# Performance work log

Hardware: AMD Instinct MI355X
Metric: run time of the kernel (lower is better)

## Reference

```python
import math
import jax, jax.numpy as jnp
import numpy as np

NHEAD = 8


def setup_inputs() -> dict:
    key = jax.random.key(0)
    ks = jax.random.split(key, 16)
    B, S, M, Ss, Ksn, D = 8, 512, 8, 16, 16, 512
    f32 = jnp.float32
    w_scale = 0.05
    return {
        "q_temporal": jax.random.normal(ks[0], (B, S, M, D), f32),
        "k_temporal": jax.random.normal(ks[1], (B, S, M, D), f32),
        "v_temporal": jax.random.normal(ks[2], (B, S, M, D), f32),
        "q_static": jax.random.normal(ks[3], (B, Ss, D), f32),
        "k_static": jax.random.normal(ks[4], (B, Ksn, D), f32),
        "v_static": jax.random.normal(ks[5], (B, Ksn, D), f32),
        "mask_temporal": jax.random.randint(ks[6], (B, S, M), 0, 2).astype(jnp.int32),
        "mask_static": jax.random.randint(ks[7], (B, Ksn), 0, 2).astype(jnp.int32),
        "Wq": jax.random.normal(ks[8], (D, D), f32) * w_scale,
        "bq": jax.random.normal(ks[9], (D,), f32) * w_scale,
        "Wk": jax.random.normal(ks[10], (D, D), f32) * w_scale,
        "bk": jax.random.normal(ks[11], (D,), f32) * w_scale,
        "Wv": jax.random.normal(ks[12], (D, D), f32) * w_scale,
        "bv": jax.random.normal(ks[13], (D,), f32) * w_scale,
        "Wo": jax.random.normal(ks[14], (D, D), f32) * w_scale,
        "bo": jax.random.normal(ks[15], (D,), f32) * w_scale,
    }


def reference(q_temporal, k_temporal, v_temporal, q_static, k_static, v_static,
              mask_temporal, mask_static, Wq, bq, Wk, bk, Wv, bv, Wo, bo):
    B, S, M, D = q_temporal.shape
    dh = D // NHEAD
    scale = 1.0 / math.sqrt(dh)
    SM = S * M

    def lin(x, W, b):
        return x @ W + b

    def h5(x):  # [B,S,M,D] -> [B,H,S,M,dh]
        b, s, m, d = x.shape
        return x.reshape(b, s, m, NHEAD, dh).transpose(0, 3, 1, 2, 4)

    def h4(x):  # [B,N,D] -> [B,H,N,dh]
        b, n, d = x.shape
        return x.reshape(b, n, NHEAD, dh).transpose(0, 2, 1, 3)

    # additive masks: 1 -> 0 (keep), 0 -> -inf
    m_t = jnp.where(mask_temporal == 1, 0.0, -jnp.inf)  # [B,S,M]
    m_s = jnp.where(mask_static == 1, 0.0, -jnp.inf)    # [B,Ks]

    # shared static-key/value heads: [B,H,Ks,dh]
    Ks_h = h4(lin(k_static, Wk, bk))
    Vs_h = h4(lin(v_static, Wv, bv))

    # ---- temporal side ----
    Qt = h5(lin(q_temporal, Wq, bq))   # [B,H,S,M,dh]
    Kt = h5(lin(k_temporal, Wk, bk))
    Vt = h5(lin(v_temporal, Wv, bv))
    qt_kt = jnp.einsum('bhsmd,bhsnd->bhsmn', Qt, Kt) * scale + m_t[:, None, :, None, :]   # [B,H,S,M,M]
    qt_ks = jnp.einsum('bhsmd,bhkd->bhsmk', Qt, Ks_h) * scale + m_s[:, None, None, None, :]  # [B,H,S,M,Ks]
    w_t = jax.nn.softmax(jnp.concatenate([qt_kt, qt_ks], axis=-1), axis=-1)  # [B,H,S,M,M+Ks]
    qkv_t = (jnp.einsum('bhsmn,bhsnd->bhsmd', w_t[..., :M], Vt)
             + jnp.einsum('bhsmk,bhkd->bhsmd', w_t[..., M:], Vs_h))          # [B,H,S,M,dh]
    out_t = lin(qkv_t.transpose(0, 2, 3, 1, 4).reshape(B, S, M, D), Wo, bo)  # [B,S,M,D]

    # ---- static side ----
    Qs = h4(lin(q_static, Wq, bq))                              # [B,H,Ss,dh]
    Kt_f = h4(lin(k_temporal.reshape(B, SM, D), Wk, bk))        # [B,H,S*M,dh]
    Vt_f = h4(lin(v_temporal.reshape(B, SM, D), Wv, bv))
    qs_kt = jnp.einsum('bhqd,bhnd->bhqn', Qs, Kt_f) * scale + m_t.reshape(B, 1, 1, SM)  # [B,H,Ss,S*M]
    qs_ks = jnp.einsum('bhqd,bhkd->bhqk', Qs, Ks_h) * scale + m_s[:, None, None, :]     # [B,H,Ss,Ks]
    w_s = jax.nn.softmax(jnp.concatenate([qs_kt, qs_ks], axis=-1), axis=-1)  # [B,H,Ss,S*M+Ks]
    qkv_s = (jnp.einsum('bhqn,bhnd->bhqd', w_s[..., :SM], Vt_f)
             + jnp.einsum('bhqk,bhkd->bhqd', w_s[..., SM:], Vs_h))           # [B,H,Ss,dh]
    Ss = qkv_s.shape[2]
    out_s = lin(qkv_s.transpose(0, 2, 1, 3).reshape(B, Ss, D), Wo, bo)       # [B,Ss,D]

    return (out_t, w_t, out_s, w_s)
```

## Files before the change

### kernel.cpp

```cpp
#include <hip/hip_runtime.h>
#include <hip/hip_bf16.h>

typedef __attribute__((ext_vector_type(8))) __bf16 bf16x8;
typedef __attribute__((ext_vector_type(4))) float f32x4;

__device__ __forceinline__ float b2f(unsigned short u) {
    unsigned int x = ((unsigned int)u) << 16;
    float f;
    __builtin_memcpy(&f, &x, 4);
    return f;
}
__device__ __forceinline__ unsigned short f2b(float f) {
    __hip_bfloat16 h = __float2bfloat16(f);
    unsigned short u;
    __builtin_memcpy(&u, &h, 2);
    return u;
}
union U4 { uint4 v; unsigned short u[8]; };

__global__ __launch_bounds__(256) void transpose512cvt(const float* __restrict__ in,
                                                       unsigned short* __restrict__ out)
{
    __shared__ float tile[32][33];
    int tx = threadIdx.x & 31, ty = threadIdx.x >> 5;
    int bx = blockIdx.x, by = blockIdx.y;
    #pragma unroll
    for (int i = 0; i < 32; i += 8)
        tile[ty + i][tx] = in[(size_t)(bx * 32 + ty + i) * 512 + by * 32 + tx];
    __syncthreads();
    #pragma unroll
    for (int i = 0; i < 32; i += 8)
        out[(size_t)(by * 32 + ty + i) * 512 + bx * 32 + tx] = f2b(tile[tx][ty + i]);
}

#define GPAD 40

template<bool AF32, int CMODE>
__global__ __launch_bounds__(256) void gemm128(
    const void* __restrict__ Av,
    const unsigned short* __restrict__ Bt,
    const float* __restrict__ bias,
    void* __restrict__ Cv,
    int M, int N)
{
    const int K = 512;
    __shared__ __align__(16) unsigned short As[128 * GPAD];
    __shared__ __align__(16) unsigned short Bs[128 * GPAD];

    int nblk = gridDim.x, bid = blockIdx.x;
    int wid = ((nblk & 7) == 0) ? ((bid & 7) * (nblk >> 3) + (bid >> 3)) : bid;
    int nt = N >> 7;
    int m0 = (wid / nt) * 128, n0 = (wid % nt) * 128;

    int t = threadIdx.x;
    int wave = t >> 6, lane = t & 63, quad = lane >> 4, l16 = lane & 15;
    int wr = wave >> 1, wc = wave & 1;

    f32x4 acc[4][4];
    #pragma unroll
    for (int i = 0; i < 4; ++i)
        #pragma unroll
        for (int j = 0; j < 4; ++j) acc[i][j] = (f32x4){0.f, 0.f, 0.f, 0.f};

    int r = t >> 1, half = (t & 1) * 16;
    const float* Ap32 = (const float*)Av + (size_t)(m0 + r) * K + half;
    const unsigned short* Ap16 = (const unsigned short*)Av + (size_t)(m0 + r) * K + half;
    const unsigned short* Bp = Bt + (size_t)(n0 + r) * K + half;

    float4 fa0, fa1, fa2, fa3;
    U4 ua0, ua1;
    uint4 fb0, fb1;

    auto LOADK = [&](int k0) {
        if constexpr (AF32) {
            const float4* p = (const float4*)(Ap32 + k0);
            fa0 = p[0]; fa1 = p[1]; fa2 = p[2]; fa3 = p[3];
        } else {
            ua0.v = *(const uint4*)(Ap16 + k0);
            ua1.v = *(const uint4*)(Ap16 + k0 + 8);
        }
        fb0 = *(const uint4*)(Bp + k0);
        fb1 = *(const uint4*)(Bp + k0 + 8);
    };
    auto STOREK = [&]() {
        U4 a0, a1;
        if constexpr (AF32) {
            a0.u[0]=f2b(fa0.x); a0.u[1]=f2b(fa0.y); a0.u[2]=f2b(fa0.z); a0.u[3]=f2b(fa0.w);
            a0.u[4]=f2b(fa1.x); a0.u[5]=f2b(fa1.y); a0.u[6]=f2b(fa1.z); a0.u[7]=f2b(fa1.w);
            a1.u[0]=f2b(fa2.x); a1.u[1]=f2b(fa2.y); a1.u[2]=f2b(fa2.z); a1.u[3]=f2b(fa2.w);
            a1.u[4]=f2b(fa3.x); a1.u[5]=f2b(fa3.y); a1.u[6]=f2b(fa3.z); a1.u[7]=f2b(fa3.w);
        } else {
            a0 = ua0; a1 = ua1;
        }
        *(uint4*)&As[r * GPAD + half] = a0.v;
        *(uint4*)&As[r * GPAD + half + 8] = a1.v;
        *(uint4*)&Bs[r * GPAD + half] = fb0;
        *(uint4*)&Bs[r * GPAD + half + 8] = fb1;
    };

    LOADK(0);
    for (int it = 0; it < 16; ++it) {
        __syncthreads();
        STOREK();
        __syncthreads();
        if (it < 15) LOADK((it + 1) * 32);
        bf16x8 af[4], bf[4];
        #pragma unroll
        for (int i = 0; i < 4; ++i)
            af[i] = *(const bf16x8*)&As[(wr * 64 + i * 16 + l16) * GPAD + quad * 8];
        #pragma unroll
        for (int j = 0; j < 4; ++j)
            bf[j] = *(const bf16x8*)&Bs[(wc * 64 + j * 16 + l16) * GPAD + quad * 8];
        #pragma unroll
        for (int i = 0; i < 4; ++i)
            #pragma unroll
            for (int j = 0; j < 4; ++j)
                acc[i][j] = __builtin_amdgcn_mfma_f32_16x16x32_bf16(af[i], bf[j], acc[i][j], 0, 0, 0);
    }
    #pragma unroll
    for (int i = 0; i < 4; ++i) {
        #pragma unroll
        for (int j = 0; j < 4; ++j) {
            int row = m0 + wr * 64 + i * 16 + quad * 4;
            int col = n0 + wc * 64 + j * 16 + l16;
            float bc = bias[col];
            #pragma unroll
            for (int ii = 0; ii < 4; ++ii) {
                float v = acc[i][j][ii] + bc;
                int R = row + ii;
                if constexpr (CMODE == 0) {
                    ((float*)Cv)[(size_t)R * N + col] = v;
                } else if constexpr (CMODE == 1) {
                    ((unsigned short*)Cv)[(size_t)R * N + col] = f2b(v);
                } else {
                    int bb = R >> 12, n = R & 4095, hh = col >> 6, d = col & 63;
                    ((unsigned short*)Cv)[(((size_t)bb * 8 + hh) * 4096 + n) * 64 + d] = f2b(v);
                }
            }
        }
    }
}

__global__ __launch_bounds__(512) void temporal_attn(
    const unsigned short* __restrict__ Qt, const unsigned short* __restrict__ KH,
    const unsigned short* __restrict__ VH, const unsigned short* __restrict__ Ksp,
    const unsigned short* __restrict__ Vsp,
    const int* __restrict__ mask_t, const int* __restrict__ mask_s,
    float* __restrict__ w_t_out, unsigned short* __restrict__ qkv_t)
{
    int blk = blockIdx.x;
    int b = blk >> 8, sp = blk & 255;
    int s0 = sp * 2;
    int t = threadIdx.x;
    int h = t >> 6, lane = t & 63, quad = lane >> 4, l16 = lane & 15;

    __shared__ __align__(16) unsigned short Vt[8][64 * 40];
    __shared__ __align__(16) unsigned short Pl[8][16 * 40];

    size_t bh = (size_t)(b * 8 + h);
    size_t tok0 = ((size_t)(b * 512 + s0)) * 8;

    {
        int r = lane & 31, dh = (lane >> 5) * 32;
        const unsigned short* src = (r < 16)
            ? VH + (bh * 4096 + (size_t)(s0 * 8 + r)) * 64 + dh
            : Vsp + ((size_t)(b * 16 + (r - 16))) * 512 + h * 64 + dh;
        U4 u[4];
        #pragma unroll
        for (int g = 0; g < 4; ++g) u[g].v = ((const uint4*)src)[g];
        unsigned short* dst = &Vt[h][0];
        #pragma unroll
        for (int g = 0; g < 4; ++g)
            #pragma unroll
            for (int ii = 0; ii < 8; ++ii)
                dst[(dh + g * 8 + ii) * 40 + r] = u[g].u[ii];
    }

    const unsigned short* qp = Qt + (tok0 + l16) * 512 + h * 64 + quad * 8;
    bf16x8 qf0 = *(const bf16x8*)qp;
    bf16x8 qf1 = *(const bf16x8*)(qp + 32);
    const unsigned short* kpt = KH + (bh * 4096 + (size_t)(s0 * 8 + l16)) * 64 + quad * 8;
    bf16x8 kt0 = *(const bf16x8*)kpt;
    bf16x8 kt1 = *(const bf16x8*)(kpt + 32);
    const unsigned short* kps = Ksp + ((size_t)(b * 16 + l16)) * 512 + h * 64 + quad * 8;
    bf16x8 ks0 = *(const bf16x8*)kps;
    bf16x8 ks1 = *(const bf16x8*)(kps + 32);

    f32x4 sc0 = (f32x4){0.f, 0.f, 0.f, 0.f};
    f32x4 sc1 = (f32x4){0.f, 0.f, 0.f, 0.f};
    sc0 = __builtin_amdgcn_mfma_f32_16x16x32_bf16(qf0, kt0, sc0, 0, 0, 0);
    sc0 = __builtin_amdgcn_mfma_f32_16x16x32_bf16(qf1, kt1, sc0, 0, 0, 0);
    sc1 = __builtin_amdgcn_mfma_f32_16x16x32_bf16(qf0, ks0, sc1, 0, 0, 0);
    sc1 = __builtin_amdgcn_mfma_f32_16x16x32_bf16(qf1, ks1, sc1, 0, 0, 0);

    float madd0 = mask_t[tok0 + l16] ? 0.f : -1e30f;
    bool v0 = ((quad < 2) == (l16 < 8));
    if (!v0) madd0 = -1e30f;
    float madd1 = mask_s[b * 16 + l16] ? 0.f : -1e30f;

    float w0[4], w1[4];
    #pragma unroll
    for (int i = 0; i < 4; ++i) {
        float a = sc0[i] * 0.125f + madd0;
        float c = sc1[i] * 0.125f + madd1;
        float mx = fmaxf(a, c);
        mx = fmaxf(mx, __shfl_xor(mx, 1));
        mx = fmaxf(mx, __shfl_xor(mx, 2));
        mx = fmaxf(mx, __shfl_xor(mx, 4));
        mx = fmaxf(mx, __shfl_xor(mx, 8));
        float e0 = __expf(a - mx), e1 = __expf(c - mx);
        float se = e0 + e1;
        se += __shfl_xor(se, 1);
        se += __shfl_xor(se, 2);
        se += __shfl_xor(se, 4);
        se += __shfl_xor(se, 8);
        float inv = 1.f / se;
        w0[i] = e0 * inv;
        w1[i] = e1 * inv;
    }

    int row0 = quad * 4;
    #pragma unroll
    for (int i = 0; i < 4; ++i) {
        int row = row0 + i;
        Pl[h][row * 40 + l16] = f2b(w0[i]);
        Pl[h][row * 40 + 16 + l16] = f2b(w1[i]);
        int s = s0 + (row >> 3), m = row & 7;
        size_t wb = ((((size_t)b * 8 + h) * 512 + s) * 8 + m) * 24;
        if (v0) w_t_out[wb + (l16 & 7)] = w0[i];
        w_t_out[wb + 8 + l16] = w1[i];
    }

    bf16x8 pa = *(const bf16x8*)&Pl[h][l16 * 40 + quad * 8];
    f32x4 oacc[4];
    #pragma unroll
    for (int j = 0; j < 4; ++j) {
        bf16x8 vb = *(const bf16x8*)&Vt[h][(j * 16 + l16) * 40 + quad * 8];
        oacc[j] = (f32x4){0.f, 0.f, 0.f, 0.f};
        oacc[j] = __builtin_amdgcn_mfma_f32_16x16x32_bf16(pa, vb, oacc[j], 0, 0, 0);
    }
    #pragma unroll
    for (int j = 0; j < 4; ++j)
        #pragma unroll
        for (int ii = 0; ii < 4; ++ii) {
            int row = quad * 4 + ii;
            qkv_t[(tok0 + row) * 512 + h * 64 + j * 16 + l16] = f2b(oacc[j][ii]);
        }
}

__global__ __launch_bounds__(256) void static_attn_s1(
    const unsigned short* __restrict__ Qsp, const unsigned short* __restrict__ KH,
    const unsigned short* __restrict__ VH, const unsigned short* __restrict__ Ksp,
    const unsigned short* __restrict__ Vsp,
    const int* __restrict__ mask_t, const int* __restrict__ mask_s,
    float* __restrict__ w_s, float* __restrict__ Ppart, float* __restrict__ Lpart)
{
    int blk = blockIdx.x;
    int bh = blk & 63, c = blk >> 6;
    int b = bh >> 3, h = bh & 7;
    __shared__ __align__(16) unsigned short Klds[32 * 72];
    __shared__ __align__(16) unsigned short Vlds[64 * 40];
    __shared__ __align__(16) unsigned short Plds[16 * 40];
    __shared__ float maskv[32];
    __shared__ float sL[2][16];
    int t = threadIdx.x, wave = t >> 6, lane = t & 63, quad = lane >> 4, l16 = lane & 15;

    bf16x8 qf0 = *(const bf16x8*)(Qsp + ((size_t)(b * 16 + l16)) * 512 + h * 64 + quad * 8);
    bf16x8 qf1 = *(const bf16x8*)(Qsp + ((size_t)(b * 16 + l16)) * 512 + h * 64 + 32 + quad * 8);

    f32x4 pacc = (f32x4){0.f, 0.f, 0.f, 0.f};
    float Lacc[4] = {0.f, 0.f, 0.f, 0.f};
    int d0 = wave * 16;
    int sub = wave >> 1;
    int sr = t >> 3, spart = t & 7;
    int s0 = c * 16, s1 = (c == 7) ? 129 : (s0 + 16);

    for (int st = s0; st < s1; ++st) {
        int key0 = st * 32;
        int kk = key0 + sr;
        uint4 kv = {0, 0, 0, 0}, vv = {0, 0, 0, 0};
        if (kk < 4096) {
            kv = *(const uint4*)(KH + (((size_t)bh) * 4096 + kk) * 64 + spart * 8);
            vv = *(const uint4*)(VH + (((size_t)bh) * 4096 + kk) * 64 + spart * 8);
        } else if (kk < 4112) {
            kv = *(const uint4*)(Ksp + ((size_t)(b * 16 + kk - 4096)) * 512 + h * 64 + spart * 8);
            vv = *(const uint4*)(Vsp + ((size_t)(b * 16 + kk - 4096)) * 512 + h * 64 + spart * 8);
        }
        __syncthreads();
        *(uint4*)&Klds[sr * 72 + spart * 8] = kv;
        {
            U4 u; u.v = vv;
            #pragma unroll
            for (int ii = 0; ii < 8; ++ii) Vlds[(spart * 8 + ii) * 40 + sr] = u.u[ii];
        }
        if (t < 32) {
            int k2 = key0 + t;
            float ma = -1e30f;
            if (k2 < 4096) ma = mask_t[b * 4096 + k2] ? 0.f : -1e30f;
            else if (k2 < 4112) ma = mask_s[b * 16 + k2 - 4096] ? 0.f : -1e30f;
            maskv[t] = ma;
        }
        __syncthreads();
        if ((wave & 1) == 0) {
            bf16x8 kf0 = *(const bf16x8*)&Klds[(sub * 16 + l16) * 72 + quad * 8];
            bf16x8 kf1 = *(const bf16x8*)&Klds[(sub * 16 + l16) * 72 + 32 + quad * 8];
            f32x4 sc = (f32x4){0.f, 0.f, 0.f, 0.f};
            sc = __builtin_amdgcn_mfma_f32_16x16x32_bf16(qf0, kf0, sc, 0, 0, 0);
            sc = __builtin_amdgcn_mfma_f32_16x16x32_bf16(qf1, kf1, sc, 0, 0, 0);
            float ma = maskv[sub * 16 + l16];
            size_t wbase = (((size_t)bh) * 16 + quad * 4) * 4112 + key0 + sub * 16 + l16;
            #pragma unroll
            for (int i = 0; i < 4; ++i) {
                float sv = sc[i] * 0.125f + ma;
                float w = __expf(sv);
                Lacc[i] += w;
                w_s[wbase + (size_t)i * 4112] = w;
                Plds[(quad * 4 + i) * 40 + sub * 16 + l16] = f2b(w);
            }
        }
        __syncthreads();
        bf16x8 pf = *(const bf16x8*)&Plds[l16 * 40 + quad * 8];
        bf16x8 vf = *(const bf16x8*)&Vlds[(d0 + l16) * 40 + quad * 8];
        pacc = __builtin_amdgcn_mfma_f32_16x16x32_bf16(pf, vf, pacc, 0, 0, 0);
    }

    if ((wave & 1) == 0) {
        #pragma unroll
        for (int i = 0; i < 4; ++i) {
            float v = Lacc[i];
            v += __shfl_xor(v, 1);
            v += __shfl_xor(v, 2);
            v += __shfl_xor(v, 4);
            v += __shfl_xor(v, 8);
            Lacc[i] = v;
        }
        if (l16 == 0) {
            #pragma unroll
            for (int i = 0; i < 4; ++i) sL[wave >> 1][quad * 4 + i] = Lacc[i];
        }
    }
    size_t pbase = ((size_t)(bh * 8 + c) * 16 + quad * 4) * 64 + d0 + l16;
    #pragma unroll
    for (int i = 0; i < 4; ++i) Ppart[pbase + (size_t)i * 64] = pacc[i];
    __syncthreads();
    if (t < 16) Lpart[(bh * 8 + c) * 16 + t] = sL[0][t] + sL[1][t];
}

__global__ __launch_bounds__(256) void static_attn_s4(
    const float* __restrict__ Ppart, const float* __restrict__ Lpart,
    float* __restrict__ w_s, unsigned short* __restrict__ qkvS)
{
    int bh = blockIdx.x, b = bh >> 3, h = bh & 7;
    __shared__ float invL[16];
    int t = threadIdx.x;
    if (t < 16) {
        float L = 0.f;
        #pragma unroll
        for (int cc = 0; cc < 8; ++cc) L += Lpart[(bh * 8 + cc) * 16 + t];
        invL[t] = 1.f / L;
    }
    __syncthreads();
    #pragma unroll
    for (int i = 0; i < 4; ++i) {
        int idx = t + i * 256;
        int q = idx >> 6, d = idx & 63;
        float s = 0.f;
        #pragma unroll
        for (int cc = 0; cc < 8; ++cc) s += Ppart[((size_t)(bh * 8 + cc) * 16 + q) * 64 + d];
        qkvS[((size_t)(b * 16 + q)) * 512 + h * 64 + d] = f2b(s * invL[q]);
    }
    size_t base = (size_t)bh * 16 * 4112;
    for (int q = 0; q < 16; ++q) {
        float il = invL[q];
        for (int kk = t; kk < 4112; kk += 256) w_s[base + q * 4112 + kk] *= il;
    }
}

extern "C" void kernel_launch(void* const* d_in, const int* in_sizes, int n_in,
                              void* d_out, int out_size, void* d_ws, size_t ws_size,
                              hipStream_t stream)
{
    const float* q_t = (const float*)d_in[0];
    const float* k_t = (const float*)d_in[1];
    const float* v_t = (const float*)d_in[2];
    const float* q_s = (const float*)d_in[3];
    const float* k_s = (const float*)d_in[4];
    const float* v_s = (const float*)d_in[5];
    const int* m_t = (const int*)d_in[6];
    const int* m_s = (const int*)d_in[7];
    const float* Wq = (const float*)d_in[8];
    const float* bq = (const float*)d_in[9];
    const float* Wk = (const float*)d_in[10];
    const float* bk = (const float*)d_in[11];
    const float* Wv = (const float*)d_in[12];
    const float* bv = (const float*)d_in[13];
    const float* Wo = (const float*)d_in[14];
    const float* bo = (const float*)d_in[15];

    char* ws = (char*)d_ws;
    size_t off = 0;
    auto alloc = [&](size_t bytes) {
        void* p = ws + off;
        off += (bytes + 255) & ~(size_t)255;
        return p;
    };
    const size_t WB = (size_t)512 * 512 * 2;
    const size_t TB = (size_t)32768 * 512 * 2;
    const size_t SB = (size_t)128 * 512 * 2;
    unsigned short* WqT = (unsigned short*)alloc(WB);
    unsigned short* WkT = (unsigned short*)alloc(WB);
    unsigned short* WvT = (unsigned short*)alloc(WB);
    unsigned short* WoT = (unsigned short*)alloc(WB);
    unsigned short* Qt   = (unsigned short*)alloc(TB);
    unsigned short* KH   = (unsigned short*)alloc(TB);
    unsigned short* VH   = (unsigned short*)alloc(TB);
    unsigned short* qkvT = (unsigned short*)alloc(TB);
    unsigned short* Qsp  = (unsigned short*)alloc(SB);
    unsigned short* Ksp  = (unsigned short*)alloc(SB);
    unsigned short* Vsp  = (unsigned short*)alloc(SB);
    unsigned short* qkvS = (unsigned short*)alloc(SB);
    float* Ppart = (float*)alloc((size_t)64 * 8 * 16 * 64 * 4);
    float* Lpart = (float*)alloc((size_t)64 * 8 * 16 * 4);

    float* out    = (float*)d_out;
    float* out_tp = out;
    float* w_t_o  = out + 16777216;
    float* out_sp = out + 23068672;
    float* w_s_o  = out + 23134208;

    transpose512cvt<<<dim3(16, 16), 256, 0, stream>>>(Wq, WqT);
    transpose512cvt<<<dim3(16, 16), 256, 0, stream>>>(Wk, WkT);
    transpose512cvt<<<dim3(16, 16), 256, 0, stream>>>(Wv, WvT);
    transpose512cvt<<<dim3(16, 16), 256, 0, stream>>>(Wo, WoT);

    gemm128<true, 1><<<dim3(1024), 256, 0, stream>>>(q_t, WqT, bq, Qt, 32768, 512);
    gemm128<true, 2><<<dim3(1024), 256, 0, stream>>>(k_t, WkT, bk, KH, 32768, 512);
    gemm128<true, 2><<<dim3(1024), 256, 0, stream>>>(v_t, WvT, bv, VH, 32768, 512);
    gemm128<true, 1><<<dim3(4),    256, 0, stream>>>(q_s, WqT, bq, Qsp, 128, 512);
    gemm128<true, 1><<<dim3(4),    256, 0, stream>>>(k_s, WkT, bk, Ksp, 128, 512);
    gemm128<true, 1><<<dim3(4),    256, 0, stream>>>(v_s, WvT, bv, Vsp, 128, 512);

    temporal_attn<<<2048, 512, 0, stream>>>(Qt, KH, VH, Ksp, Vsp, m_t, m_s, w_t_o, qkvT);
    static_attn_s1<<<512, 256, 0, stream>>>(Qsp, KH, VH, Ksp, Vsp, m_t, m_s, w_s_o, Ppart, Lpart);
    static_attn_s4<<<64, 256, 0, stream>>>(Ppart, Lpart, w_s_o, qkvS);

    gemm128<false, 0><<<dim3(1024), 256, 0, stream>>>(qkvT, WoT, bo, out_tp, 32768, 512);
    gemm128<false, 0><<<dim3(4),    256, 0, stream>>>(qkvS, WoT, bo, out_sp, 128, 512);
}
```

Baseline: 589.5 us.

## Batch QKV projection GEMMs and weight transposes into single launches, add register prefetch

Merges the four weight transpose kernels into one launch using blockIdx.z, and the three temporal (and three static) QKV projection GEMMs into one launch each using blockIdx.y to select a parameter set. The GEMM main loop now keeps two register staging buffers so global loads run two K-steps ahead of the MFMA compute. This cuts launch overhead and fills the GPU better for the tiny static GEMMs. In exchange, the output mode becomes a runtime branch instead of a template constant, and the extra staging registers may lower occupancy.

```diff
diff --git a/kernel.cpp b/kernel.cpp
--- a/kernel.cpp
+++ b/kernel.cpp
@@ -18,9 +18,17 @@
 }
 union U4 { uint4 v; unsigned short u[8]; };
 
-__global__ __launch_bounds__(256) void transpose512cvt(const float* __restrict__ in,
-                                                       unsigned short* __restrict__ out)
-{
+__global__ __launch_bounds__(256) void transpose512cvt4(
+    const float* __restrict__ i0, const float* __restrict__ i1,
+    const float* __restrict__ i2, const float* __restrict__ i3,
+    unsigned short* __restrict__ o0, unsigned short* __restrict__ o1,
+    unsigned short* __restrict__ o2, unsigned short* __restrict__ o3)
+{
+    const float* in = i0;
+    unsigned short* out = o0;
+    if (blockIdx.z == 1) { in = i1; out = o1; }
+    else if (blockIdx.z == 2) { in = i2; out = o2; }
+    else if (blockIdx.z == 3) { in = i3; out = o3; }
     __shared__ float tile[32][33];
     int tx = threadIdx.x & 31, ty = threadIdx.x >> 5;
     int bx = blockIdx.x, by = blockIdx.y;
@@ -35,14 +43,22 @@
 
 #define GPAD 40
 
-template<bool AF32, int CMODE>
+struct GemmSet {
+    const void* A;
+    const unsigned short* B;
+    const float* bias;
+    void* C;
+    int cmode;
+};
+
+template<bool AF32>
 __global__ __launch_bounds__(256) void gemm128(
-    const void* __restrict__ Av,
-    const unsigned short* __restrict__ Bt,
-    const float* __restrict__ bias,
-    void* __restrict__ Cv,
-    int M, int N)
-{
+    GemmSet s0, GemmSet s1, GemmSet s2, int M, int N)
+{
+    GemmSet S = s0;
+    if (blockIdx.y == 1) S = s1;
+    else if (blockIdx.y == 2) S = s2;
+
     const int K = 512;
     __shared__ __align__(16) unsigned short As[128 * GPAD];
     __shared__ __align__(16) unsigned short Bs[128 * GPAD];
@@ -63,15 +79,14 @@
         for (int j = 0; j < 4; ++j) acc[i][j] = (f32x4){0.f, 0.f, 0.f, 0.f};
 
     int r = t >> 1, half = (t & 1) * 16;
-    const float* Ap32 = (const float*)Av + (size_t)(m0 + r) * K + half;
-    const unsigned short* Ap16 = (const unsigned short*)Av + (size_t)(m0 + r) * K + half;
-    const unsigned short* Bp = Bt + (size_t)(n0 + r) * K + half;
-
-    float4 fa0, fa1, fa2, fa3;
-    U4 ua0, ua1;
-    uint4 fb0, fb1;
-
-    auto LOADK = [&](int k0) {
+    const float* Ap32 = (const float*)S.A + (size_t)(m0 + r) * K + half;
+    const unsigned short* Ap16 = (const unsigned short*)S.A + (size_t)(m0 + r) * K + half;
+    const unsigned short* Bp = S.B + (size_t)(n0 + r) * K + half;
+
+    float4 fa0, fa1, fa2, fa3; U4 ua0, ua1; uint4 fb0, fb1;
+    float4 ga0, ga1, ga2, ga3; U4 va0, va1; uint4 gb0, gb1;
+
+    auto LOAD0 = [&](int k0) {
         if constexpr (AF32) {
             const float4* p = (const float4*)(Ap32 + k0);
             fa0 = p[0]; fa1 = p[1]; fa2 = p[2]; fa3 = p[3];
@@ -82,28 +97,44 @@
         fb0 = *(const uint4*)(Bp + k0);
         fb1 = *(const uint4*)(Bp + k0 + 8);
     };
-    auto STOREK = [&]() {
+    auto LOAD1 = [&](int k0) {
+        if constexpr (AF32) {
+            const float4* p = (const float4*)(Ap32 + k0);
+            ga0 = p[0]; ga1 = p[1]; ga2 = p[2]; ga3 = p[3];
+        } else {
+            va0.v = *(const uint4*)(Ap16 + k0);
+            va1.v = *(const uint4*)(Ap16 + k0 + 8);
+        }
+        gb0 = *(const uint4*)(Bp + k0);
+        gb1 = *(const uint4*)(Bp + k0 + 8);
+    };
+    auto STORE0 = [&]() {
         U4 a0, a1;
         if constexpr (AF32) {
             a0.u[0]=f2b(fa0.x); a0.u[1]=f2b(fa0.y); a0.u[2]=f2b(fa0.z); a0.u[3]=f2b(fa0.w);
             a0.u[4]=f2b(fa1.x); a0.u[5]=f2b(fa1.y); a0.u[6]=f2b(fa1.z); a0.u[7]=f2b(fa1.w);
             a1.u[0]=f2b(fa2.x); a1.u[1]=f2b(fa2.y); a1.u[2]=f2b(fa2.z); a1.u[3]=f2b(fa2.w);
             a1.u[4]=f2b(fa3.x); a1.u[5]=f2b(fa3.y); a1.u[6]=f2b(fa3.z); a1.u[7]=f2b(fa3.w);
-        } else {
-            a0 = ua0; a1 = ua1;
-        }
+        } else { a0 = ua0; a1 = ua1; }
         *(uint4*)&As[r * GPAD + half] = a0.v;
         *(uint4*)&As[r * GPAD + half + 8] = a1.v;
         *(uint4*)&Bs[r * GPAD + half] = fb0;
         *(uint4*)&Bs[r * GPAD + half + 8] = fb1;
     };
-
-    LOADK(0);
-    for (int it = 0; it < 16; ++it) {
-        __syncthreads();
-        STOREK();
-        __syncthreads();
-        if (it < 15) LOADK((it + 1) * 32);
+    auto STORE1 = [&]() {
+        U4 a0, a1;
+        if constexpr (AF32) {
+            a0.u[0]=f2b(ga0.x); a0.u[1]=f2b(ga0.y); a0.u[2]=f2b(ga0.z); a0.u[3]=f2b(ga0.w);
+            a0.u[4]=f2b(ga1.x); a0.u[5]=f2b(ga1.y); a0.u[6]=f2b(ga1.z); a0.u[7]=f2b(ga1.w);
+            a1.u[0]=f2b(ga2.x); a1.u[1]=f2b(ga2.y); a1.u[2]=f2b(ga2.z); a1.u[3]=f2b(ga2.w);
+            a1.u[4]=f2b(ga3.x); a1.u[5]=f2b(ga3.y); a1.u[6]=f2b(ga3.z); a1.u[7]=f2b(ga3.w);
+        } else { a0 = va0; a1 = va1; }
+        *(uint4*)&As[r * GPAD + half] = a0.v;
+        *(uint4*)&As[r * GPAD + half + 8] = a1.v;
+        *(uint4*)&Bs[r * GPAD + half] = gb0;
+        *(uint4*)&Bs[r * GPAD + half + 8] = gb1;
+    };
+    auto COMPUTE = [&]() {
         bf16x8 af[4], bf[4];
         #pragma unroll
         for (int i = 0; i < 4; ++i)
@@ -116,25 +147,42 @@
             #pragma unroll
             for (int j = 0; j < 4; ++j)
                 acc[i][j] = __builtin_amdgcn_mfma_f32_16x16x32_bf16(af[i], bf[j], acc[i][j], 0, 0, 0);
-    }
+    };
+
+    LOAD0(0);
+    LOAD1(32);
+    for (int it = 0; it < 16; it += 2) {
+        __syncthreads();
+        STORE0();
+        __syncthreads();
+        if (it + 2 < 16) LOAD0((it + 2) * 32);
+        COMPUTE();
+        __syncthreads();
+        STORE1();
+        __syncthreads();
+        if (it + 3 < 16) LOAD1((it + 3) * 32);
+        COMPUTE();
+    }
+
+    int cmode = S.cmode;
     #pragma unroll
     for (int i = 0; i < 4; ++i) {
         #pragma unroll
         for (int j = 0; j < 4; ++j) {
             int row = m0 + wr * 64 + i * 16 + quad * 4;
             int col = n0 + wc * 64 + j * 16 + l16;
-            float bc = bias[col];
+            float bc = S.bias[col];
             #pragma unroll
             for (int ii = 0; ii < 4; ++ii) {
                 float v = acc[i][j][ii] + bc;
                 int R = row + ii;
-                if constexpr (CMODE == 0) {
-                    ((float*)Cv)[(size_t)R * N + col] = v;
-                } else if constexpr (CMODE == 1) {
-                    ((unsigned short*)Cv)[(size_t)R * N + col] = f2b(v);
+                if (cmode == 0) {
+                    ((float*)S.C)[(size_t)R * N + col] = v;
+                } else if (cmode == 1) {
+                    ((unsigned short*)S.C)[(size_t)R * N + col] = f2b(v);
                 } else {
                     int bb = R >> 12, n = R & 4095, hh = col >> 6, d = col & 63;
-                    ((unsigned short*)Cv)[(((size_t)bb * 8 + hh) * 4096 + n) * 64 + d] = f2b(v);
+                    ((unsigned short*)S.C)[(((size_t)bb * 8 + hh) * 4096 + n) * 64 + d] = f2b(v);
                 }
             }
         }
@@ -428,22 +476,24 @@
     float* out_sp = out + 23068672;
     float* w_s_o  = out + 23134208;
 
-    transpose512cvt<<<dim3(16, 16), 256, 0, stream>>>(Wq, WqT);
-    transpose512cvt<<<dim3(16, 16), 256, 0, stream>>>(Wk, WkT);
-    transpose512cvt<<<dim3(16, 16), 256, 0, stream>>>(Wv, WvT);
-    transpose512cvt<<<dim3(16, 16), 256, 0, stream>>>(Wo, WoT);
-
-    gemm128<true, 1><<<dim3(1024), 256, 0, stream>>>(q_t, WqT, bq, Qt, 32768, 512);
-    gemm128<true, 2><<<dim3(1024), 256, 0, stream>>>(k_t, WkT, bk, KH, 32768, 512);
-    gemm128<true, 2><<<dim3(1024), 256, 0, stream>>>(v_t, WvT, bv, VH, 32768, 512);
-    gemm128<true, 1><<<dim3(4),    256, 0, stream>>>(q_s, WqT, bq, Qsp, 128, 512);
-    gemm128<true, 1><<<dim3(4),    256, 0, stream>>>(k_s, WkT, bk, Ksp, 128, 512);
-    gemm128<true, 1><<<dim3(4),    256, 0, stream>>>(v_s, WvT, bv, Vsp, 128, 512);
+    transpose512cvt4<<<dim3(16, 16, 4), 256, 0, stream>>>(Wq, Wk, Wv, Wo, WqT, WkT, WvT, WoT);
+
+    GemmSet gq  = { q_t,  WqT, bq, Qt,   1 };
+    GemmSet gk  = { k_t,  WkT, bk, KH,   2 };
+    GemmSet gv  = { v_t,  WvT, bv, VH,   2 };
+    GemmSet gqs = { q_s,  WqT, bq, Qsp,  1 };
+    GemmSet gks = { k_s,  WkT, bk, Ksp,  1 };
+    GemmSet gvs = { v_s,  WvT, bv, Vsp,  1 };
+    GemmSet got = { qkvT, WoT, bo, out_tp, 0 };
+    GemmSet gos = { qkvS, WoT, bo, out_sp, 0 };
+
+    gemm128<true><<<dim3(1024, 3), 256, 0, stream>>>(gq, gk, gv, 32768, 512);
+    gemm128<true><<<dim3(4, 3),    256, 0, stream>>>(gqs, gks, gvs, 128, 512);
 
     temporal_attn<<<2048, 512, 0, stream>>>(Qt, KH, VH, Ksp, Vsp, m_t, m_s, w_t_o, qkvT);
     static_attn_s1<<<512, 256, 0, stream>>>(Qsp, KH, VH, Ksp, Vsp, m_t, m_s, w_s_o, Ppart, Lpart);
     static_attn_s4<<<64, 256, 0, stream>>>(Ppart, Lpart, w_s_o, qkvS);
 
-    gemm128<false, 0><<<dim3(1024), 256, 0, stream>>>(qkvT, WoT, bo, out_tp, 32768, 512);
-    gemm128<false, 0><<<dim3(4),    256, 0, stream>>>(qkvS, WoT, bo, out_sp, 128, 512);
-}
+    gemm128<false><<<dim3(1024, 1), 256, 0, stream>>>(got, got, got, 32768, 512);
+    gemm128<false><<<dim3(4, 1),    256, 0, stream>>>(gos, gos, gos, 128, 512);
+}
```

Measured after the change: 581.3 us. No clear change (-1.4%).
